# Kernel tuning notes

Measured on AMD Instinct MI355X. Metric: run time of the kernel, lower is better.

The kernel has to match this reference:

```python
import jax, jax.numpy as jnp
import numpy as np

N_NODES = 100000
N_EDGES = 1600000
IN_FEATS = 64
HIDDEN = 64
TOPO_DIM = 16
NUM_CLASSES = 4
NUM_GRAPHS = 64


def setup_inputs() -> dict:
    key = jax.random.key(0)
    ks = jax.random.split(key, 10)
    x = jax.random.normal(ks[0], (N_NODES, IN_FEATS), dtype=jnp.float32)
    edge_index = jax.random.randint(ks[1], (2, N_EDGES), 0, N_NODES, dtype=jnp.int64)
    batch = jnp.sort(jax.random.randint(ks[2], (N_NODES,), 0, NUM_GRAPHS, dtype=jnp.int64))
    topo = jax.random.normal(ks[3], (NUM_GRAPHS, TOPO_DIM), dtype=jnp.float32)
    # GCNConv weights (glorot-ish scale) and biases
    W1 = jax.random.normal(ks[4], (IN_FEATS, HIDDEN), dtype=jnp.float32) / np.sqrt(IN_FEATS)
    b1 = jnp.zeros((HIDDEN,), dtype=jnp.float32)
    W2 = jax.random.normal(ks[5], (HIDDEN, HIDDEN), dtype=jnp.float32) / np.sqrt(HIDDEN)
    b2 = jnp.zeros((HIDDEN,), dtype=jnp.float32)
    Wlin = jax.random.normal(ks[6], (HIDDEN + TOPO_DIM, NUM_CLASSES), dtype=jnp.float32) / np.sqrt(HIDDEN + TOPO_DIM)
    blin = jnp.zeros((NUM_CLASSES,), dtype=jnp.float32)
    return {"x": x, "edge_index": edge_index, "batch": batch, "topo": topo,
            "W1": W1, "b1": b1, "W2": W2, "b2": b2, "Wlin": Wlin, "blin": blin}


def _gcn_conv(x, W, b, src, dst, deg_inv_sqrt):
    # PyG GCNConv: add self-loops, symmetric normalization D^-1/2 (A+I) D^-1/2, then linear.
    xw = x @ W                                   # [N, H]
    norm = deg_inv_sqrt[src] * deg_inv_sqrt[dst]  # [E]
    msgs = xw[src] * norm[:, None]               # gather + scale, [E, H]
    agg = jax.ops.segment_sum(msgs, dst, num_segments=x.shape[0])
    # self-loop contribution: norm_ii = deg_inv_sqrt[i]^2
    agg = agg + xw * (deg_inv_sqrt * deg_inv_sqrt)[:, None]
    return agg + b


def reference(x, edge_index, batch, topo, W1, b1, W2, b2, Wlin, blin):
    src, dst = edge_index[0], edge_index[1]
    n = x.shape[0]
    # degree including self-loop
    deg = jax.ops.segment_sum(jnp.ones_like(dst, dtype=x.dtype), dst, num_segments=n) + 1.0
    deg_inv_sqrt = jax.lax.rsqrt(deg)
    h = jax.nn.relu(_gcn_conv(x, W1, b1, src, dst, deg_inv_sqrt))
    # F.dropout(p=0.5, training=False) -> identity at inference
    h = jax.nn.relu(_gcn_conv(h, W2, b2, src, dst, deg_inv_sqrt))
    # global mean pool over graphs
    sums = jax.ops.segment_sum(h, batch, num_segments=NUM_GRAPHS)
    counts = jax.ops.segment_sum(jnp.ones((n,), dtype=h.dtype), batch, num_segments=NUM_GRAPHS)
    g = sums / jnp.maximum(counts, 1.0)[:, None]  # [G, H]
    gtopo = jnp.concatenate([g, topo], axis=1)    # [G, H + topo_dim]
    return gtopo @ Wlin + blin
```

## Files before the change

### kernel.cpp

```cpp
#include <hip/hip_runtime.h>
#include <hip/hip_bf16.h>

#define NGRAPH  64
#define TOPO_D  16
#define NBLK    512
#define MAXB    512
#define GROWS   8

typedef float v2f __attribute__((ext_vector_type(2)));

static __device__ __forceinline__ unsigned f2bf(float f) {
    unsigned u = __float_as_uint(f);
    return (u + 0x7FFFu + ((u >> 16) & 1u)) >> 16;
}
static __device__ __forceinline__ float bf_lo(unsigned u) { return __uint_as_float(u << 16); }
static __device__ __forceinline__ float bf_hi(unsigned u) { return __uint_as_float(u & 0xFFFF0000u); }

static __device__ __forceinline__ void gemm_rows_bf(
        const float* __restrict__ X, const float* Wreg,
        unsigned short* __restrict__ Abf, int row0, int N, int lane) {
    #pragma unroll
    for (int j = 0; j < GROWS; ++j) {
        int row = row0 + j;
        int rc = min(row, N - 1);
        const float* xr = X + (size_t)rc * 64;
        float a0 = 0.f, a1 = 0.f, a2 = 0.f, a3 = 0.f;
        #pragma unroll
        for (int k = 0; k < 64; k += 4) {
            a0 = fmaf(xr[k],     Wreg[k],     a0);
            a1 = fmaf(xr[k + 1], Wreg[k + 1], a1);
            a2 = fmaf(xr[k + 2], Wreg[k + 2], a2);
            a3 = fmaf(xr[k + 3], Wreg[k + 3], a3);
        }
        float acc = (a0 + a1) + (a2 + a3);
        if (row < N)
            Abf[(size_t)row * 64 + lane] = (unsigned short)f2bf(acc);
    }
}

__global__ __launch_bounds__(256) void hybrid_gemm_hist_kernel(
        const float* __restrict__ X, const float* __restrict__ W,
        unsigned short* __restrict__ Abf,
        const int* __restrict__ dst, int* __restrict__ bhist,
        const int* __restrict__ batch, int* __restrict__ gstart,
        float* __restrict__ gsum,
        int N, int E, int Gg, int nb2, int CE) {
    __shared__ int hist[MAXB];
    int t = threadIdx.x;
    if ((int)blockIdx.x < Gg) {
        int lane = t & 63;
        float Wreg[64];
        #pragma unroll
        for (int k = 0; k < 64; ++k) Wreg[k] = W[k * 64 + lane];
        int wave = __builtin_amdgcn_readfirstlane(blockIdx.x * 4 + (t >> 6));
        gemm_rows_bf(X, Wreg, Abf, wave * GROWS, N, lane);
    } else if ((int)blockIdx.x < Gg + NBLK) {
        int blk = blockIdx.x - Gg;
        for (int i = t; i < nb2; i += 256) hist[i] = 0;
        __syncthreads();
        int e0 = blk * CE, e1 = min(e0 + CE, E);
        for (int e = e0 + t; e < e1; e += 256) atomicAdd(&hist[dst[e] >> 8], 1);
        __syncthreads();
        for (int i = t; i < nb2; i += 256) bhist[blk * nb2 + i] = hist[i];
    } else if ((int)blockIdx.x == Gg + NBLK) {
        int g = t;
        if (g <= NGRAPH) {
            int lo = 0, hi = N;
            while (lo < hi) {
                int mid = (lo + hi) >> 1;
                if (batch[mid] < g) lo = mid + 1; else hi = mid;
            }
            gstart[g] = lo;
        }
    } else {
        for (int i = t; i < NGRAPH * 64; i += 256) gsum[i] = 0.f;
    }
}

__global__ __launch_bounds__(256) void scan_cols_kernel(
        int* __restrict__ bhist, int* __restrict__ ctot, int nb2) {
    __shared__ int sd[256];
    int c = blockIdx.x;
    int t = threadIdx.x;
    int v0 = bhist[t * nb2 + c];
    int v1 = bhist[(t + 256) * nb2 + c];
    int tsum = v0 + v1;
    sd[t] = tsum; __syncthreads();
    for (int off = 1; off < 256; off <<= 1) {
        int u = (t >= off) ? sd[t - off] : 0;
        __syncthreads();
        sd[t] += u;
        __syncthreads();
    }
    int excl = sd[t] - tsum;
    bhist[t * nb2 + c] = excl;
    bhist[(t + 256) * nb2 + c] = excl + v0;
    if (t == 255) ctot[c] = sd[255];
}

__global__ __launch_bounds__(256) void scatter_sorted_kernel(
        const int* __restrict__ src, const int* __restrict__ dst,
        const int* __restrict__ bhist, const int* __restrict__ ctot,
        unsigned* __restrict__ ebuf, int E, int nb2, int CE) {
    __shared__ int sd[256];
    __shared__ int cur[MAXB];
    int blk = blockIdx.x, t = threadIdx.x;
    int v0 = (t < nb2) ? ctot[t] : 0;
    int v1 = (t + 256 < nb2) ? ctot[t + 256] : 0;
    int tsum = v0 + v1;
    sd[t] = tsum; __syncthreads();
    for (int off = 1; off < 256; off <<= 1) {
        int u = (t >= off) ? sd[t - off] : 0;
        __syncthreads();
        sd[t] += u;
        __syncthreads();
    }
    int excl = sd[t] - tsum;
    if (t < nb2)       cur[t]       = bhist[blk * nb2 + t] + excl;
    if (t + 256 < nb2) cur[t + 256] = bhist[blk * nb2 + t + 256] + excl + v0;
    __syncthreads();
    int e0 = blk * CE, e1 = min(e0 + CE, E);
    for (int e = e0 + t; e < e1; e += 256) {
        int d = dst[e];
        int pos = atomicAdd(&cur[d >> 8], 1);
        ebuf[pos] = ((unsigned)src[e] << 8) | (unsigned)(d & 255);
    }
}

__global__ __launch_bounds__(256) void build_csr_kernel(
        const unsigned* __restrict__ ebuf, const int* __restrict__ ctot,
        int* __restrict__ col, int* __restrict__ rowptr,
        int* __restrict__ degi, float* __restrict__ dis,
        const unsigned* __restrict__ Abf32, unsigned* __restrict__ A8, int N) {
    __shared__ int cnt[256];
    __shared__ int loff[256];
    __shared__ float disS[256];
    __shared__ int redS[256];
    int b = blockIdx.x, t = threadIdx.x;
    int part = 0;
    for (int i = t; i < b; i += 256) part += ctot[i];
    redS[t] = part; __syncthreads();
    for (int off = 128; off > 0; off >>= 1) {
        if (t < off) redS[t] += redS[t + off];
        __syncthreads();
    }
    int e0 = redS[0];
    int e1 = e0 + ctot[b];
    cnt[t] = 0; __syncthreads();
    for (int i = e0 + t; i < e1; i += 256) atomicAdd(&cnt[ebuf[i] & 255u], 1);
    __syncthreads();
    int v = cnt[t];
    loff[t] = v; __syncthreads();
    for (int off = 1; off < 256; off <<= 1) {
        int u = (t >= off) ? loff[t - off] : 0;
        __syncthreads();
        loff[t] += u;
        __syncthreads();
    }
    int excl = loff[t] - v;
    int node = b * 256 + t;
    float ds = rsqrtf((float)v + 1.0f);
    disS[t] = ds;
    if (node < N) {
        degi[node]   = v;
        dis[node]    = ds;
        rowptr[node] = e0 + excl;
    }
    __syncthreads();
    cnt[t] = excl;
    __syncthreads();
    for (int i = e0 + t; i < e1; i += 256) {
        unsigned p = ebuf[i];
        int pos = atomicAdd(&cnt[p & 255u], 1);
        col[e0 + pos] = (int)(p >> 8);
    }
    int base8 = b * 256 * 16;
    for (int i = t; i < 256 * 16; i += 256) {
        int r = i >> 4;
        int dwo = i & 15;
        int nd = b * 256 + r;
        if (nd < N) {
            float d2 = disS[r];
            unsigned u0 = Abf32[(size_t)nd * 32 + dwo * 2];
            unsigned u1 = Abf32[(size_t)nd * 32 + dwo * 2 + 1];
            int dw = __builtin_amdgcn_cvt_pk_fp8_f32(bf_lo(u0) * d2, bf_hi(u0) * d2, 0, false);
            dw = __builtin_amdgcn_cvt_pk_fp8_f32(bf_lo(u1) * d2, bf_hi(u1) * d2, dw, true);
            A8[base8 + i] = (unsigned)dw;
        }
    }
}

#define CVT_ACC(vv) do { \
    v2f f0_ = __builtin_amdgcn_cvt_pk_f32_fp8((vv).x, false); acc[0] += f0_.x; acc[1] += f0_.y; \
    v2f f1_ = __builtin_amdgcn_cvt_pk_f32_fp8((vv).x, true);  acc[2] += f1_.x; acc[3] += f1_.y; \
    v2f f2_ = __builtin_amdgcn_cvt_pk_f32_fp8((vv).y, false); acc[4] += f2_.x; acc[5] += f2_.y; \
    v2f f3_ = __builtin_amdgcn_cvt_pk_f32_fp8((vv).y, true);  acc[6] += f3_.x; acc[7] += f3_.y; \
} while (0)

static __device__ __forceinline__ void gather_node(
        const unsigned* __restrict__ A8, const int* __restrict__ col,
        int beg, int deg, int node, int f8, float acc[8]) {
    const char* Abase = (const char*)A8 + f8 * 8;
    uint2 an = *(const uint2*)(Abase + ((size_t)node << 6));
    v2f a0 = __builtin_amdgcn_cvt_pk_f32_fp8(an.x, false);
    v2f a1 = __builtin_amdgcn_cvt_pk_f32_fp8(an.x, true);
    v2f a2 = __builtin_amdgcn_cvt_pk_f32_fp8(an.y, false);
    v2f a3 = __builtin_amdgcn_cvt_pk_f32_fp8(an.y, true);
    acc[0] = a0.x; acc[1] = a0.y; acc[2] = a1.x; acc[3] = a1.y;
    acc[4] = a2.x; acc[5] = a2.y; acc[6] = a3.x; acc[7] = a3.y;
    int j = 0;
    for (; j + 8 <= deg; j += 8) {
        int s0 = col[beg + j]     << 6;
        int s1 = col[beg + j + 1] << 6;
        int s2 = col[beg + j + 2] << 6;
        int s3 = col[beg + j + 3] << 6;
        int s4 = col[beg + j + 4] << 6;
        int s5 = col[beg + j + 5] << 6;
        int s6 = col[beg + j + 6] << 6;
        int s7 = col[beg + j + 7] << 6;
        uint2 v0 = *(const uint2*)(Abase + s0);
        uint2 v1 = *(const uint2*)(Abase + s1);
        uint2 v2 = *(const uint2*)(Abase + s2);
        uint2 v3 = *(const uint2*)(Abase + s3);
        uint2 v4 = *(const uint2*)(Abase + s4);
        uint2 v5 = *(const uint2*)(Abase + s5);
        uint2 v6 = *(const uint2*)(Abase + s6);
        uint2 v7 = *(const uint2*)(Abase + s7);
        CVT_ACC(v0); CVT_ACC(v1); CVT_ACC(v2); CVT_ACC(v3);
        CVT_ACC(v4); CVT_ACC(v5); CVT_ACC(v6); CVT_ACC(v7);
    }
    for (; j + 4 <= deg; j += 4) {
        int s0 = col[beg + j]     << 6;
        int s1 = col[beg + j + 1] << 6;
        int s2 = col[beg + j + 2] << 6;
        int s3 = col[beg + j + 3] << 6;
        uint2 v0 = *(const uint2*)(Abase + s0);
        uint2 v1 = *(const uint2*)(Abase + s1);
        uint2 v2 = *(const uint2*)(Abase + s2);
        uint2 v3 = *(const uint2*)(Abase + s3);
        CVT_ACC(v0); CVT_ACC(v1); CVT_ACC(v2); CVT_ACC(v3);
    }
    for (; j < deg; ++j) {
        int s = col[beg + j] << 6;
        uint2 v = *(const uint2*)(Abase + s);
        CVT_ACC(v);
    }
}

__global__ __launch_bounds__(256) void pull_csr_kernel(
        const unsigned* __restrict__ A8, unsigned* __restrict__ C8,
        const int* __restrict__ rowptr, const int* __restrict__ degi,
        const float* __restrict__ dis, const float* __restrict__ bias,
        const int* __restrict__ col, int N) {
    int wave = (blockIdx.x * blockDim.x + threadIdx.x) >> 6;
    int lane = threadIdx.x & 63;
    int i = lane >> 3;
    int f8 = lane & 7;
    int node = wave * 8 + i;
    bool valid = node < N;
    if (!valid) node = N - 1;
    int deg = degi[node];
    int beg = rowptr[node];
    float acc[8];
    gather_node(A8, col, beg, deg, node, f8, acc);
    float d = dis[node];
    float4 b0 = ((const float4*)bias)[f8 * 2];
    float4 b1 = ((const float4*)bias)[f8 * 2 + 1];
    float r0 = fmaxf(d * acc[0] + b0.x, 0.f);
    float r1 = fmaxf(d * acc[1] + b0.y, 0.f);
    float r2 = fmaxf(d * acc[2] + b0.z, 0.f);
    float r3 = fmaxf(d * acc[3] + b0.w, 0.f);
    float r4 = fmaxf(d * acc[4] + b1.x, 0.f);
    float r5 = fmaxf(d * acc[5] + b1.y, 0.f);
    float r6 = fmaxf(d * acc[6] + b1.z, 0.f);
    float r7 = fmaxf(d * acc[7] + b1.w, 0.f);
    if (valid) {
        int p0 = __builtin_amdgcn_cvt_pk_fp8_f32(d * r0, d * r1, 0, false);
        p0 = __builtin_amdgcn_cvt_pk_fp8_f32(d * r2, d * r3, p0, true);
        int p1 = __builtin_amdgcn_cvt_pk_fp8_f32(d * r4, d * r5, 0, false);
        p1 = __builtin_amdgcn_cvt_pk_fp8_f32(d * r6, d * r7, p1, true);
        uint2 o; o.x = (unsigned)p0; o.y = (unsigned)p1;
        *(uint2*)((char*)C8 + ((size_t)node << 6) + (f8 << 3)) = o;
    }
}

__global__ __launch_bounds__(512) void pull2_pool_kernel(
        const unsigned* __restrict__ C8, const int* __restrict__ rowptr,
        const int* __restrict__ degi, const float* __restrict__ dis,
        const float* __restrict__ bias, const int* __restrict__ col,
        const int* __restrict__ batch, const float* __restrict__ W2,
        float* __restrict__ gsum, int N) {
    __shared__ float w2s[4096];
    __shared__ __align__(16) float sred[64][72];
    __shared__ float red[8][65];
    int t = threadIdx.x;
    ((float4*)w2s)[t]       = ((const float4*)W2)[t];
    ((float4*)w2s)[t + 512] = ((const float4*)W2)[t + 512];
    int wave = (blockIdx.x * blockDim.x + t) >> 6;
    int lane = t & 63;
    int w = t >> 6;
    int i = lane >> 3;
    int f8 = lane & 7;
    int node = wave * 8 + i;
    bool valid = node < N;
    if (!valid) node = N - 1;
    int deg = degi[node];
    int beg = rowptr[node];
    float acc[8];
    gather_node(C8, col, beg, deg, node, f8, acc);
    float* sp = &sred[w * 8 + i][f8 * 8];
    sp[0] = acc[0]; sp[1] = acc[1]; sp[2] = acc[2]; sp[3] = acc[3];
    sp[4] = acc[4]; sp[5] = acc[5]; sp[6] = acc[6]; sp[7] = acc[7];
    __syncthreads();
    float g0 = 0.f, g1 = 0.f, g2 = 0.f, g3 = 0.f, g4 = 0.f, g5 = 0.f, g6 = 0.f, g7 = 0.f;
    #pragma unroll
    for (int kc = 0; kc < 16; ++kc) {
        float wa = w2s[(kc * 4 + 0) * 64 + lane];
        float wb = w2s[(kc * 4 + 1) * 64 + lane];
        float wc = w2s[(kc * 4 + 2) * 64 + lane];
        float wd = w2s[(kc * 4 + 3) * 64 + lane];
        float4 sv;
        sv = *(const float4*)&sred[w * 8 + 0][kc * 4];
        g0 = fmaf(sv.x, wa, fmaf(sv.y, wb, fmaf(sv.z, wc, fmaf(sv.w, wd, g0))));
        sv = *(const float4*)&sred[w * 8 + 1][kc * 4];
        g1 = fmaf(sv.x, wa, fmaf(sv.y, wb, fmaf(sv.z, wc, fmaf(sv.w, wd, g1))));
        sv = *(const float4*)&sred[w * 8 + 2][kc * 4];
        g2 = fmaf(sv.x, wa, fmaf(sv.y, wb, fmaf(sv.z, wc, fmaf(sv.w, wd, g2))));
        sv = *(const float4*)&sred[w * 8 + 3][kc * 4];
        g3 = fmaf(sv.x, wa, fmaf(sv.y, wb, fmaf(sv.z, wc, fmaf(sv.w, wd, g3))));
        sv = *(const float4*)&sred[w * 8 + 4][kc * 4];
        g4 = fmaf(sv.x, wa, fmaf(sv.y, wb, fmaf(sv.z, wc, fmaf(sv.w, wd, g4))));
        sv = *(const float4*)&sred[w * 8 + 5][kc * 4];
        g5 = fmaf(sv.x, wa, fmaf(sv.y, wb, fmaf(sv.z, wc, fmaf(sv.w, wd, g5))));
        sv = *(const float4*)&sred[w * 8 + 6][kc * 4];
        g6 = fmaf(sv.x, wa, fmaf(sv.y, wb, fmaf(sv.z, wc, fmaf(sv.w, wd, g6))));
        sv = *(const float4*)&sred[w * 8 + 7][kc * 4];
        g7 = fmaf(sv.x, wa, fmaf(sv.y, wb, fmaf(sv.z, wc, fmaf(sv.w, wd, g7))));
    }
    int base = (blockIdx.x * 8 + w) * 8;
    float d0 = dis[min(base + 0, N - 1)];
    float d1 = dis[min(base + 1, N - 1)];
    float d2 = dis[min(base + 2, N - 1)];
    float d3 = dis[min(base + 3, N - 1)];
    float d4 = dis[min(base + 4, N - 1)];
    float d5 = dis[min(base + 5, N - 1)];
    float d6 = dis[min(base + 6, N - 1)];
    float d7 = dis[min(base + 7, N - 1)];
    float bf = bias[lane];
    float h0 = fmaxf(fmaf(d0, g0, bf), 0.f);
    float h1 = fmaxf(fmaf(d1, g1, bf), 0.f);
    float h2 = fmaxf(fmaf(d2, g2, bf), 0.f);
    float h3 = fmaxf(fmaf(d3, g3, bf), 0.f);
    float h4 = fmaxf(fmaf(d4, g4, bf), 0.f);
    float h5 = fmaxf(fmaf(d5, g5, bf), 0.f);
    float h6 = fmaxf(fmaf(d6, g6, bf), 0.f);
    float h7 = fmaxf(fmaf(d7, g7, bf), 0.f);
    if (base + 0 >= N) h0 = 0.f;
    if (base + 1 >= N) h1 = 0.f;
    if (base + 2 >= N) h2 = 0.f;
    if (base + 3 >= N) h3 = 0.f;
    if (base + 4 >= N) h4 = 0.f;
    if (base + 5 >= N) h5 = 0.f;
    if (base + 6 >= N) h6 = 0.f;
    if (base + 7 >= N) h7 = 0.f;
    int nodeA = blockIdx.x * 64;
    int gA = batch[min(nodeA, N - 1)];
    int gB = batch[min(nodeA + 63, N - 1)];
    if (gA == gB) {
        red[w][lane] = h0 + h1 + h2 + h3 + h4 + h5 + h6 + h7;
        __syncthreads();
        if (t < 64) {
            float s = red[0][t] + red[1][t] + red[2][t] + red[3][t]
                    + red[4][t] + red[5][t] + red[6][t] + red[7][t];
            unsafeAtomicAdd(&gsum[gA * 64 + t], s);
        }
    } else {
        int q0 = batch[min(base + 0, N - 1)]; unsafeAtomicAdd(&gsum[q0 * 64 + lane], h0);
        int q1 = batch[min(base + 1, N - 1)]; unsafeAtomicAdd(&gsum[q1 * 64 + lane], h1);
        int q2 = batch[min(base + 2, N - 1)]; unsafeAtomicAdd(&gsum[q2 * 64 + lane], h2);
        int q3 = batch[min(base + 3, N - 1)]; unsafeAtomicAdd(&gsum[q3 * 64 + lane], h3);
        int q4 = batch[min(base + 4, N - 1)]; unsafeAtomicAdd(&gsum[q4 * 64 + lane], h4);
        int q5 = batch[min(base + 5, N - 1)]; unsafeAtomicAdd(&gsum[q5 * 64 + lane], h5);
        int q6 = batch[min(base + 6, N - 1)]; unsafeAtomicAdd(&gsum[q6 * 64 + lane], h6);
        int q7 = batch[min(base + 7, N - 1)]; unsafeAtomicAdd(&gsum[q7 * 64 + lane], h7);
    }
}

__global__ __launch_bounds__(256) void head_kernel(
        const float* __restrict__ gsum, const int* __restrict__ gstart,
        const float* __restrict__ topo, const float* __restrict__ Wlin,
        const float* __restrict__ blin, float* __restrict__ out) {
    int t = threadIdx.x;
    int g = t >> 2;
    int c = t & 3;
    float cntf = (float)(gstart[g + 1] - gstart[g]);
    float inv = 1.0f / fmaxf(cntf, 1.0f);
    float v = blin[c];
    #pragma unroll
    for (int f = 0; f < 64; ++f) v += gsum[g * 64 + f] * inv * Wlin[f * 4 + c];
    #pragma unroll
    for (int t2 = 0; t2 < TOPO_D; ++t2) v += topo[g * TOPO_D + t2] * Wlin[(64 + t2) * 4 + c];
    out[g * 4 + c] = v;
}

extern "C" void kernel_launch(void* const* d_in, const int* in_sizes, int n_in,
                              void* d_out, int out_size, void* d_ws, size_t ws_size,
                              hipStream_t stream) {
    const float* x     = (const float*)d_in[0];
    const int*   ei    = (const int*)d_in[1];
    const int*   batch = (const int*)d_in[2];
    const float* topo  = (const float*)d_in[3];
    const float* W1    = (const float*)d_in[4];
    const float* b1    = (const float*)d_in[5];
    const float* W2    = (const float*)d_in[6];
    const float* b2    = (const float*)d_in[7];
    const float* Wlin  = (const float*)d_in[8];
    const float* blin  = (const float*)d_in[9];
    float* out = (float*)d_out;

    const int N = in_sizes[0] / 64;
    const int E = in_sizes[1] / 2;
    const int* src = ei;
    const int* dst = ei + E;
    const int nb2 = (N + 255) / 256;
    const int CE  = (E + NBLK - 1) / NBLK;

    char* ws = (char*)d_ws;
    size_t off = 0;
    unsigned short* Abf = (unsigned short*)(ws + off); off += (size_t)N * 64 * 2;
    unsigned* A8     = (unsigned*)(ws + off); off += (size_t)N * 64;
    unsigned* C8     = (unsigned*)(ws + off); off += (size_t)N * 64;
    int*      col    = (int*)     (ws + off); off += (size_t)E * 4;
    unsigned* ebuf   = (unsigned*)(ws + off); off += (size_t)E * 4;
    int*      bhist  = (int*)     (ws + off); off += (size_t)NBLK * nb2 * 4;
    int*      ctot   = (int*)     (ws + off); off += (size_t)(nb2 + 8) * 4;
    int*      rowptr = (int*)     (ws + off); off += (size_t)(N + 1) * 4;
    int*      degi   = (int*)     (ws + off); off += (size_t)N * 4;
    float*    dis    = (float*)   (ws + off); off += (size_t)N * 4;
    int*      gstart = (int*)     (ws + off); off += (size_t)(NGRAPH + 8) * 4;
    float*    gsum   = (float*)   (ws + off); off += (size_t)NGRAPH * 64 * 4;

    const int nWaves = (N + GROWS - 1) / GROWS;
    const int Gg = (nWaves + 3) / 4;
    hybrid_gemm_hist_kernel<<<Gg + NBLK + 2, 256, 0, stream>>>(
        x, W1, Abf, dst, bhist, batch, gstart, gsum, N, E, Gg, nb2, CE);
    scan_cols_kernel<<<nb2, 256, 0, stream>>>(bhist, ctot, nb2);
    scatter_sorted_kernel<<<NBLK, 256, 0, stream>>>(src, dst, bhist, ctot, ebuf, E, nb2, CE);
    build_csr_kernel<<<nb2, 256, 0, stream>>>(ebuf, ctot, col, rowptr, degi, dis,
                                              (const unsigned*)Abf, A8, N);

    int pullBlocks = ((N + 7) / 8 + 3) / 4;
    pull_csr_kernel<<<pullBlocks, 256, 0, stream>>>(A8, C8, rowptr, degi, dis, b1, col, N);

    int pull2Blocks = (N + 63) / 64;
    pull2_pool_kernel<<<pull2Blocks, 512, 0, stream>>>(C8, rowptr, degi, dis, b2, col,
                                                       batch, W2, gsum, N);

    head_kernel<<<1, 256, 0, stream>>>(gsum, gstart, topo, Wlin, blin, out);
}
```

Measured before the change: 211.0 us.

## Split first-layer GEMM across hist, scan and scatter kernels

```diff
diff --git a/kernel.cpp b/kernel.cpp
--- a/kernel.cpp
+++ b/kernel.cpp
@@ -38,31 +38,37 @@
     }
 }
 
-__global__ __launch_bounds__(256) void hybrid_gemm_hist_kernel(
+static __device__ __forceinline__ void gemm1_block(
+        const float* __restrict__ X, const float* __restrict__ W,
+        unsigned short* __restrict__ Abf, int gb, int N, int t) {
+    int lane = t & 63;
+    float Wreg[64];
+    #pragma unroll
+    for (int k = 0; k < 64; ++k) Wreg[k] = W[k * 64 + lane];
+    int wave = __builtin_amdgcn_readfirstlane(gb * 4 + (t >> 6));
+    gemm_rows_bf(X, Wreg, Abf, wave * GROWS, N, lane);
+}
+
+__global__ __launch_bounds__(256) void hist_gemm_kernel(
         const float* __restrict__ X, const float* __restrict__ W,
         unsigned short* __restrict__ Abf,
         const int* __restrict__ dst, int* __restrict__ bhist,
         const int* __restrict__ batch, int* __restrict__ gstart,
         float* __restrict__ gsum,
-        int N, int E, int Gg, int nb2, int CE) {
+        int N, int E, int GA, int nb2, int CE) {
     __shared__ int hist[MAXB];
     int t = threadIdx.x;
-    if ((int)blockIdx.x < Gg) {
-        int lane = t & 63;
-        float Wreg[64];
-        #pragma unroll
-        for (int k = 0; k < 64; ++k) Wreg[k] = W[k * 64 + lane];
-        int wave = __builtin_amdgcn_readfirstlane(blockIdx.x * 4 + (t >> 6));
-        gemm_rows_bf(X, Wreg, Abf, wave * GROWS, N, lane);
-    } else if ((int)blockIdx.x < Gg + NBLK) {
-        int blk = blockIdx.x - Gg;
+    if ((int)blockIdx.x < GA) {
+        gemm1_block(X, W, Abf, blockIdx.x, N, t);
+    } else if ((int)blockIdx.x < GA + NBLK) {
+        int blk = blockIdx.x - GA;
         for (int i = t; i < nb2; i += 256) hist[i] = 0;
         __syncthreads();
         int e0 = blk * CE, e1 = min(e0 + CE, E);
         for (int e = e0 + t; e < e1; e += 256) atomicAdd(&hist[dst[e] >> 8], 1);
         __syncthreads();
         for (int i = t; i < nb2; i += 256) bhist[blk * nb2 + i] = hist[i];
-    } else if ((int)blockIdx.x == Gg + NBLK) {
+    } else if ((int)blockIdx.x == GA + NBLK) {
         int g = t;
         if (g <= NGRAPH) {
             int lo = 0, hi = N;
@@ -77,11 +83,18 @@
     }
 }
 
-__global__ __launch_bounds__(256) void scan_cols_kernel(
-        int* __restrict__ bhist, int* __restrict__ ctot, int nb2) {
+__global__ __launch_bounds__(256) void scan_gemm_kernel(
+        int* __restrict__ bhist, int* __restrict__ ctot,
+        const float* __restrict__ X, const float* __restrict__ W,
+        unsigned short* __restrict__ Abf,
+        int N, int GA, int nb2) {
     __shared__ int sd[256];
+    int t = threadIdx.x;
+    if ((int)blockIdx.x >= nb2) {
+        gemm1_block(X, W, Abf, (int)blockIdx.x - nb2 + GA, N, t);
+        return;
+    }
     int c = blockIdx.x;
-    int t = threadIdx.x;
     int v0 = bhist[t * nb2 + c];
     int v1 = bhist[(t + 256) * nb2 + c];
     int tsum = v0 + v1;
@@ -98,13 +111,21 @@
     if (t == 255) ctot[c] = sd[255];
 }
 
-__global__ __launch_bounds__(256) void scatter_sorted_kernel(
+__global__ __launch_bounds__(256) void scatter_gemm_kernel(
         const int* __restrict__ src, const int* __restrict__ dst,
         const int* __restrict__ bhist, const int* __restrict__ ctot,
-        unsigned* __restrict__ ebuf, int E, int nb2, int CE) {
+        unsigned* __restrict__ ebuf,
+        const float* __restrict__ X, const float* __restrict__ W,
+        unsigned short* __restrict__ Abf,
+        int N, int E, int GAB, int nb2, int CE) {
     __shared__ int sd[256];
     __shared__ int cur[MAXB];
-    int blk = blockIdx.x, t = threadIdx.x;
+    int t = threadIdx.x;
+    if ((int)blockIdx.x >= NBLK) {
+        gemm1_block(X, W, Abf, (int)blockIdx.x - NBLK + GAB, N, t);
+        return;
+    }
+    int blk = blockIdx.x;
     int v0 = (t < nb2) ? ctot[t] : 0;
     int v1 = (t + 256 < nb2) ? ctot[t + 256] : 0;
     int tsum = v0 + v1;
@@ -442,10 +463,14 @@
 
     const int nWaves = (N + GROWS - 1) / GROWS;
     const int Gg = (nWaves + 3) / 4;
-    hybrid_gemm_hist_kernel<<<Gg + NBLK + 2, 256, 0, stream>>>(
-        x, W1, Abf, dst, bhist, batch, gstart, gsum, N, E, Gg, nb2, CE);
-    scan_cols_kernel<<<nb2, 256, 0, stream>>>(bhist, ctot, nb2);
-    scatter_sorted_kernel<<<NBLK, 256, 0, stream>>>(src, dst, bhist, ctot, ebuf, E, nb2, CE);
+    const int GA = (Gg + 2) / 3;
+    const int GB = GA;
+    const int GC = Gg - GA - GB;
+    hist_gemm_kernel<<<GA + NBLK + 2, 256, 0, stream>>>(
+        x, W1, Abf, dst, bhist, batch, gstart, gsum, N, E, GA, nb2, CE);
+    scan_gemm_kernel<<<nb2 + GB, 256, 0, stream>>>(bhist, ctot, x, W1, Abf, N, GA, nb2);
+    scatter_gemm_kernel<<<NBLK + GC, 256, 0, stream>>>(src, dst, bhist, ctot, ebuf,
+                                                       x, W1, Abf, N, E, GA + GB, nb2, CE);
     build_csr_kernel<<<nb2, 256, 0, stream>>>(ebuf, ctot, col, rowptr, degi, dis,
                                               (const unsigned*)Abf, A8, N);
 
```

Measured after the change: 208.4 us. About the same (-1.2%).
